# Kernel optimization log

Measured on AMD Instinct MI355X. Metric: run time of the kernel, lower is better.

The kernel has to match this reference:

```python
import jax, jax.numpy as jnp
import numpy as np


def setup_inputs() -> dict:
    key = jax.random.key(0)
    ks = jax.random.split(key, 7)
    B, T, D, H, L, O = 64, 512, 1024, 1024, 4, 256
    s = 1.0 / np.sqrt(H)
    return {
        "x": jax.random.normal(ks[0], (B, T, D), dtype=jnp.float32),
        "Wih": jax.random.normal(ks[1], (L, 4 * H, D), dtype=jnp.float32) * s,
        "Whh": jax.random.normal(ks[2], (L, 4 * H, H), dtype=jnp.float32) * s,
        "bih": jax.random.normal(ks[3], (L, 4 * H), dtype=jnp.float32) * s,
        "bhh": jax.random.normal(ks[4], (L, 4 * H), dtype=jnp.float32) * s,
        "fc_w": jax.random.normal(ks[5], (O, H), dtype=jnp.float32) * s,
        "fc_b": jax.random.normal(ks[6], (O,), dtype=jnp.float32) * s,
    }


def reference(x, Wih, Whh, bih, bhh, fc_w, fc_b):
    B, T, D = x.shape
    L, fourH, H = Whh.shape[0], Whh.shape[1], Whh.shape[2]

    def step(carry, xt):
        h, c = carry  # each [L, B, H]
        inp = xt      # [B, D]
        new_h, new_c = [], []
        for i in range(L):  # fixed small layer loop
            gates = (inp @ Wih[i].T + bih[i] + h[i] @ Whh[i].T + bhh[i])  # [B, 4H]
            ig, fg, gg, og = jnp.split(gates, 4, axis=-1)
            ig, fg, og = jax.nn.sigmoid(ig), jax.nn.sigmoid(fg), jax.nn.sigmoid(og)
            gg = jnp.tanh(gg)
            ci = fg * c[i] + ig * gg
            hi = og * jnp.tanh(ci)
            new_h.append(hi)
            new_c.append(ci)
            inp = hi
        return (jnp.stack(new_h), jnp.stack(new_c)), None

    h0 = jnp.zeros((L, B, H), dtype=x.dtype)
    c0 = jnp.zeros((L, B, H), dtype=x.dtype)
    xt_seq = jnp.swapaxes(x, 0, 1)  # [T, B, D]
    (h, c), _ = jax.lax.scan(step, (h0, c0), xt_seq)
    return h[-1] @ fc_w.T + fc_b  # [B, O]
```

## Files before the change

### kernel.cpp

```cpp
#include <hip/hip_runtime.h>
#include <stdint.h>

typedef __attribute__((ext_vector_type(8))) short short8;
typedef __attribute__((ext_vector_type(4))) float floatx4;
typedef unsigned short ushort_t;

#define NB 256
#define NT 512
constexpr int B_ = 64, T_ = 512, D_ = 1024, H_ = 1024, O_ = 256;

constexpr size_t WS_SLOTS = 0;
constexpr size_t WS_MODE  = 4096;
constexpr size_t WS_HBUF  = 8192;
constexpr size_t WS_NEED  = WS_HBUF + (size_t)4*4*B_*H_*2;

constexpr int LDS_BYTES = 131072;

__device__ __forceinline__ float bs2f(ushort_t s){
  union { unsigned u; float f; } v; v.u = ((unsigned)s) << 16; return v.f;
}
__device__ __forceinline__ ushort_t f2bs(float f){
  union { float f; unsigned u; } v; v.f = f;
  unsigned r = (v.u + 0x7fffu + ((v.u >> 16) & 1u)) >> 16;
  return (ushort_t)r;
}
__device__ __forceinline__ float sigf(float x){ return 1.f/(1.f + __expf(-x)); }
__device__ __forceinline__ float tanh_f(float x){ return 1.f - 2.f/(__expf(2.f*x) + 1.f); }
__device__ __forceinline__ short8 ldb8(const ushort_t* p){ return *(const short8*)p; }
__device__ __forceinline__ short8 cvt8v(const float* p){
  floatx4 a = *(const floatx4*)p;
  floatx4 b = *(const floatx4*)(p + 4);
  short8 r;
  #pragma unroll
  for (int j = 0; j < 4; ++j){ r[j] = (short)f2bs(a[j]); r[j+4] = (short)f2bs(b[j]); }
  return r;
}

__device__ __forceinline__ void waitge_sys(unsigned* p, int tgt){
  while ((int)__hip_atomic_load(p, __ATOMIC_RELAXED, __HIP_MEMORY_SCOPE_SYSTEM) < tgt)
    __builtin_amdgcn_s_sleep(2);
  asm volatile("" ::: "memory");
}
__device__ __forceinline__ void st_dword_sys(void* p, unsigned v){
  asm volatile("global_store_dword %0, %1, off sc0 sc1"
               :: "v"((uintptr_t)p), "v"(v) : "memory");
}
template<int AUX>
__device__ __forceinline__ void gl2lds16(const void* g, void* l){
  __builtin_amdgcn_global_load_lds(
      (const __attribute__((address_space(1))) unsigned*)g,
      (__attribute__((address_space(3))) unsigned*)l, 16, 0, AUX);
}

__global__ void sniff_init(const ushort_t* __restrict__ fcb_u,
                           unsigned* __restrict__ slots, unsigned* __restrict__ mode){
  __shared__ int cnt;
  if (threadIdx.x == 0) cnt = 0;
  __syncthreads();
  slots[threadIdx.x] = 0u;
  unsigned u = fcb_u[threadIdx.x];
  unsigned e = (u >> 7) & 0xFFu;
  if (e >= 0x89u) atomicAdd(&cnt, 1);
  __syncthreads();
  if (threadIdx.x == 0) *mode = (cnt >= 4) ? 1u : 0u;
}

__global__ __launch_bounds__(NT, 2)
void lstm_pipe(const void* __restrict__ xv,   const void* __restrict__ Wihv,
               const void* __restrict__ Whhv, const void* __restrict__ bihv,
               const void* __restrict__ bhhv, const void* __restrict__ fcwv,
               const void* __restrict__ fcbv, void* __restrict__ outv,
               ushort_t* __restrict__ hbuf, unsigned* __restrict__ slots,
               const unsigned* __restrict__ modep)
{
  extern __shared__ char lds_raw[];
  const int tid  = threadIdx.x;
  const int bx   = blockIdx.x;
  const int lane = tid & 63;
  const int wv   = tid >> 6;
  const int q    = lane >> 4;
  const int l15  = lane & 15;
  const int wg   = wv >> 1;
  const int kh   = wv & 1;
  const int s7   = l15 & 7;
  const int layer = bx >> 6;
  const int slice = bx & 63;
  const int jbase = slice * 16;

  const unsigned md = *modep;
  const bool f32in  = (md == 1u);
  const float*    xF = (const float*)xv;
  const ushort_t* xB = (const ushort_t*)xv;

  short8 wih_r[16], whh_r[16];
  {
    const size_t wrow = (size_t)layer*4*H_ + (size_t)wg*H_ + jbase + l15;
    const size_t koff = (size_t)kh*512 + q*8;
    if (f32in){
      const float* wi = (const float*)Wihv + wrow*D_ + koff;
      const float* wh = (const float*)Whhv + wrow*H_ + koff;
      #pragma unroll
      for (int kk = 0; kk < 16; ++kk){
        wih_r[kk] = cvt8v(wi + kk*32);
        whh_r[kk] = cvt8v(wh + kk*32);
      }
    } else {
      const ushort_t* wi = (const ushort_t*)Wihv + wrow*D_ + koff;
      const ushort_t* wh = (const ushort_t*)Whhv + wrow*H_ + koff;
      #pragma unroll
      for (int kk = 0; kk < 16; ++kk){
        wih_r[kk] = ldb8(wi + kk*32);
        whh_r[kk] = ldb8(wh + kk*32);
      }
    }
  }

  const int pb = tid >> 3;
  const int pj = tid & 7;
  float bsum[4][2];
  {
    #pragma unroll
    for (int g = 0; g < 4; ++g){
      const size_t idx = (size_t)layer*4*H_ + (size_t)g*H_ + jbase + 2*pj;
      if (f32in){
        bsum[g][0] = ((const float*)bihv)[idx]   + ((const float*)bhhv)[idx];
        bsum[g][1] = ((const float*)bihv)[idx+1] + ((const float*)bhhv)[idx+1];
      } else {
        bsum[g][0] = bs2f(((const ushort_t*)bihv)[idx])   + bs2f(((const ushort_t*)bhhv)[idx]);
        bsum[g][1] = bs2f(((const ushort_t*)bihv)[idx+1]) + bs2f(((const ushort_t*)bhhv)[idx+1]);
      }
    }
  }
  float c2[2] = {0.f, 0.f};

  #define GEMM_STEP(WREG) do {                                                 \
    const short8* Ap_ = (const short8*)lds_raw;                                \
    _Pragma("unroll")                                                          \
    for (int kk = 0; kk < 16; ++kk){                                           \
      const int csw = ((kh<<6) + q + (kk<<2)) ^ s7;                            \
      short8 a0 = Ap_[(size_t)(l15+ 0)*128 + csw];                             \
      short8 a1 = Ap_[(size_t)(l15+16)*128 + csw];                             \
      short8 a2 = Ap_[(size_t)(l15+32)*128 + csw];                             \
      short8 a3 = Ap_[(size_t)(l15+48)*128 + csw];                             \
      acc[0] = __builtin_amdgcn_mfma_f32_16x16x32_bf16(a0, WREG[kk], acc[0], 0,0,0); \
      acc[1] = __builtin_amdgcn_mfma_f32_16x16x32_bf16(a1, WREG[kk], acc[1], 0,0,0); \
      acc[2] = __builtin_amdgcn_mfma_f32_16x16x32_bf16(a2, WREG[kk], acc[2], 0,0,0); \
      acc[3] = __builtin_amdgcn_mfma_f32_16x16x32_bf16(a3, WREG[kk], acc[3], 0,0,0); \
    }                                                                          \
  } while(0)

  for (int t = 0; t < T_; ++t){
    if (t > 0 && tid < 64)                    waitge_sys(&slots[layer*64 + tid], t + 1);
    if (layer < 3 && t >= 3 && tid >= 64 && tid < 128)
                                              waitge_sys(&slots[(layer+1)*64 + (tid-64)], t - 2);
    __syncthreads();

    floatx4 acc[4];
    #pragma unroll
    for (int mt = 0; mt < 4; ++mt) acc[mt] = floatx4{0.f,0.f,0.f,0.f};

    if (t > 0){
      const char* src = (const char*)(hbuf + ((size_t)layer*4 + ((t+3)&3))*(size_t)(B_*H_));
      #pragma unroll
      for (int it = 0; it < 16; ++it){
        const int d = it*NT + tid;
        const int r = d >> 7, c = d & 127, cc = c ^ (r & 7);
        gl2lds16<0x11>(src + (size_t)r*2048 + (size_t)cc*16, lds_raw + (size_t)d*16);
      }
      asm volatile("s_waitcnt vmcnt(0)" ::: "memory");
      __syncthreads();
      GEMM_STEP(whh_r);
    }

    if (layer > 0 && tid < 64) waitge_sys(&slots[(layer-1)*64 + tid], t + 2);
    __syncthreads();

    if (layer == 0){
      if (f32in){
        #pragma unroll 4
        for (int it = 0; it < 16; ++it){
          const int d = it*NT + tid;
          const int r = d >> 7, c = d & 127, cc = c ^ (r & 7);
          const float* sp = xF + ((size_t)r*T_ + t)*D_ + (size_t)cc*8;
          floatx4 A0 = *(const floatx4*)sp, A1 = *(const floatx4*)(sp + 4);
          short8 v;
          #pragma unroll
          for (int j2 = 0; j2 < 4; ++j2){ v[j2] = (short)f2bs(A0[j2]); v[j2+4] = (short)f2bs(A1[j2]); }
          *(short8*)(lds_raw + (size_t)d*16) = v;
        }
      } else {
        const char* srcx = (const char*)xB;
        #pragma unroll
        for (int it = 0; it < 16; ++it){
          const int d = it*NT + tid;
          const int r = d >> 7, c = d & 127, cc = c ^ (r & 7);
          gl2lds16<0>(srcx + (((size_t)r*T_ + t)*D_ + (size_t)cc*8)*2, lds_raw + (size_t)d*16);
        }
      }
    } else {
      const char* srch = (const char*)(hbuf + ((size_t)(layer-1)*4 + (t&3))*(size_t)(B_*H_));
      #pragma unroll
      for (int it = 0; it < 16; ++it){
        const int d = it*NT + tid;
        const int r = d >> 7, c = d & 127, cc = c ^ (r & 7);
        gl2lds16<0x11>(srch + (size_t)r*2048 + (size_t)cc*16, lds_raw + (size_t)d*16);
      }
    }
    asm volatile("s_waitcnt vmcnt(0)" ::: "memory");
    __syncthreads();
    GEMM_STEP(wih_r);
    __syncthreads();

    {
      float* xch = (float*)lds_raw;
      #pragma unroll
      for (int mt = 0; mt < 4; ++mt)
        #pragma unroll
        for (int r = 0; r < 4; ++r)
          xch[((size_t)(wg*2 + kh)*64 + mt*16 + q*4 + r)*18 + l15] = acc[mt][r];
    }
    __syncthreads();

    {
      const float* xch = (const float*)lds_raw;
      float hv[2];
      #pragma unroll
      for (int u = 0; u < 2; ++u){
        const int j = 2*pj + u;
        #define XG(g) (xch[((size_t)((g)*2+0)*64 + pb)*18 + j] + xch[((size_t)((g)*2+1)*64 + pb)*18 + j])
        float ig = sigf  (XG(0) + bsum[0][u]);
        float fg = sigf  (XG(1) + bsum[1][u]);
        float gg = tanh_f(XG(2) + bsum[2][u]);
        float og = sigf  (XG(3) + bsum[3][u]);
        #undef XG
        float cn = fg*c2[u] + ig*gg;
        c2[u] = cn;
        hv[u] = og*tanh_f(cn);
      }
      unsigned pack = (unsigned)f2bs(hv[0]) | ((unsigned)f2bs(hv[1]) << 16);
      ushort_t* hw = hbuf + ((size_t)layer*4 + (t&3))*(size_t)(B_*H_) + (size_t)pb*H_ + jbase + 2*pj;
      st_dword_sys(hw, pack);
    }
    asm volatile("s_waitcnt vmcnt(0)" ::: "memory");
    __syncthreads();
    if (tid == 0)
      __hip_atomic_store(&slots[layer*64 + slice], (unsigned)(t + 2),
                         __ATOMIC_RELAXED, __HIP_MEMORY_SCOPE_SYSTEM);
  }

  if (bx < B_){
    if (tid < 64) waitge_sys(&slots[3*64 + tid], T_ + 1);
    __syncthreads();
    const char* hr = (const char*)(hbuf + (((size_t)3*4 + ((T_-1)&3))*B_ + bx)*(size_t)H_);
    if (tid < 128) gl2lds16<0x11>(hr + (size_t)tid*16, lds_raw + (size_t)tid*16);
    asm volatile("s_waitcnt vmcnt(0)" ::: "memory");
    __syncthreads();
    if (tid < O_){
      const int b = bx, o = tid;
      const short8* hh = (const short8*)lds_raw;
      if (f32in){
        float acc = ((const float*)fcbv)[o];
        const float* wr = (const float*)fcwv + (size_t)o*H_;
        for (int k8 = 0; k8 < H_/8; ++k8){
          short8 h8 = hh[k8];
          #pragma unroll
          for (int u = 0; u < 8; ++u) acc += bs2f((ushort_t)h8[u]) * wr[k8*8 + u];
        }
        ((float*)outv)[(size_t)b*O_ + o] = acc;
      } else {
        float acc = bs2f(((const ushort_t*)fcbv)[o]);
        const ushort_t* wr = (const ushort_t*)fcwv + (size_t)o*H_;
        for (int k8 = 0; k8 < H_/8; ++k8){
          short8 h8 = hh[k8];
          short8 w8 = ldb8(wr + k8*8);
          #pragma unroll
          for (int u = 0; u < 8; ++u) acc += bs2f((ushort_t)h8[u]) * bs2f((ushort_t)w8[u]);
        }
        ((ushort_t*)outv)[(size_t)b*O_ + o] = f2bs(acc);
      }
    }
  }
  #undef GEMM_STEP
}

extern "C" void kernel_launch(void* const* d_in, const int* in_sizes, int n_in,
                              void* d_out, int out_size, void* d_ws, size_t ws_size,
                              hipStream_t stream){
  static bool attr_done = false;
  if (!attr_done){
    hipFuncSetAttribute(reinterpret_cast<const void*>(&lstm_pipe),
                        hipFuncAttributeMaxDynamicSharedMemorySize, LDS_BYTES);
    attr_done = true;
  }
  char* ws = (char*)d_ws;
  unsigned* slots = (unsigned*)(ws + WS_SLOTS);
  unsigned* mode  = (unsigned*)(ws + WS_MODE);
  ushort_t* hbuf  = (ushort_t*)(ws + WS_HBUF);

  sniff_init<<<1, 256, 0, stream>>>((const ushort_t*)d_in[6], slots, mode);
  lstm_pipe<<<NB, NT, LDS_BYTES, stream>>>(d_in[0], d_in[1], d_in[2], d_in[3], d_in[4],
                                           d_in[5], d_in[6], d_out, hbuf, slots, mode);
}
```

Baseline: 11.47 ms.

## Load h operands straight from global into registers, split K across all waves

Each of the 8 waves now owns a 128-wide K slice across all four gates, not a (gate, K-half) pair. Activation fragments are read directly from hbuf and x into registers with system-scope atomic loads, replacing staging through LDS. Partial sums from all waves are reduced in LDS before the gate math, and all dependency waits happen together at the top of each step. This removes the LDS staging copies and extra barriers per timestep, at the cost of an 8-way LDS reduction, more LDS, and uncached system-scope global loads on the critical path.

```diff
diff --git a/kernel.cpp b/kernel.cpp
--- a/kernel.cpp
+++ b/kernel.cpp
@@ -3,7 +3,9 @@
 
 typedef __attribute__((ext_vector_type(8))) short short8;
 typedef __attribute__((ext_vector_type(4))) float floatx4;
+typedef __attribute__((ext_vector_type(2))) float float2v;
 typedef unsigned short ushort_t;
+typedef unsigned long long ull_t;
 
 #define NB 256
 #define NT 512
@@ -12,9 +14,8 @@
 constexpr size_t WS_SLOTS = 0;
 constexpr size_t WS_MODE  = 4096;
 constexpr size_t WS_HBUF  = 8192;
-constexpr size_t WS_NEED  = WS_HBUF + (size_t)4*4*B_*H_*2;
-
-constexpr int LDS_BYTES = 131072;
+
+constexpr int LDS_BYTES = 147456;
 
 __device__ __forceinline__ float bs2f(ushort_t s){
   union { unsigned u; float f; } v; v.u = ((unsigned)s) << 16; return v.f;
@@ -27,13 +28,15 @@
 __device__ __forceinline__ float sigf(float x){ return 1.f/(1.f + __expf(-x)); }
 __device__ __forceinline__ float tanh_f(float x){ return 1.f - 2.f/(__expf(2.f*x) + 1.f); }
 __device__ __forceinline__ short8 ldb8(const ushort_t* p){ return *(const short8*)p; }
-__device__ __forceinline__ short8 cvt8v(const float* p){
-  floatx4 a = *(const floatx4*)p;
-  floatx4 b = *(const floatx4*)(p + 4);
-  short8 r;
-  #pragma unroll
-  for (int j = 0; j < 4; ++j){ r[j] = (short)f2bs(a[j]); r[j+4] = (short)f2bs(b[j]); }
-  return r;
+
+__device__ __forceinline__ unsigned cvtpk(float lo, float hi){
+  unsigned r; asm("v_cvt_pk_bf16_f32 %0, %1, %2" : "=v"(r) : "v"(lo), "v"(hi)); return r;
+}
+__device__ __forceinline__ short8 cvt8pk(floatx4 a, floatx4 b){
+  union { unsigned u[4]; short8 s; } c;
+  c.u[0] = cvtpk(a[0], a[1]); c.u[1] = cvtpk(a[2], a[3]);
+  c.u[2] = cvtpk(b[0], b[1]); c.u[3] = cvtpk(b[2], b[3]);
+  return c.s;
 }
 
 __device__ __forceinline__ void waitge_sys(unsigned* p, int tgt){
@@ -77,12 +80,9 @@
   const int tid  = threadIdx.x;
   const int bx   = blockIdx.x;
   const int lane = tid & 63;
-  const int wv   = tid >> 6;
+  const int w    = tid >> 6;
   const int q    = lane >> 4;
   const int l15  = lane & 15;
-  const int wg   = wv >> 1;
-  const int kh   = wv & 1;
-  const int s7   = l15 & 7;
   const int layer = bx >> 6;
   const int slice = bx & 63;
   const int jbase = slice * 16;
@@ -92,25 +92,23 @@
   const float*    xF = (const float*)xv;
   const ushort_t* xB = (const ushort_t*)xv;
 
-  short8 wih_r[16], whh_r[16];
+  short8 wih_r[4][4], whh_r[4][4];
   {
-    const size_t wrow = (size_t)layer*4*H_ + (size_t)wg*H_ + jbase + l15;
-    const size_t koff = (size_t)kh*512 + q*8;
-    if (f32in){
-      const float* wi = (const float*)Wihv + wrow*D_ + koff;
-      const float* wh = (const float*)Whhv + wrow*H_ + koff;
-      #pragma unroll
-      for (int kk = 0; kk < 16; ++kk){
-        wih_r[kk] = cvt8v(wi + kk*32);
-        whh_r[kk] = cvt8v(wh + kk*32);
-      }
-    } else {
-      const ushort_t* wi = (const ushort_t*)Wihv + wrow*D_ + koff;
-      const ushort_t* wh = (const ushort_t*)Whhv + wrow*H_ + koff;
-      #pragma unroll
-      for (int kk = 0; kk < 16; ++kk){
-        wih_r[kk] = ldb8(wi + kk*32);
-        whh_r[kk] = ldb8(wh + kk*32);
+    #pragma unroll
+    for (int g = 0; g < 4; ++g){
+      const size_t row = (size_t)layer*4*H_ + (size_t)g*H_ + jbase + l15;
+      #pragma unroll
+      for (int kl = 0; kl < 4; ++kl){
+        const size_t koff = (size_t)w*128 + kl*32 + q*8;
+        if (f32in){
+          const float* wi = (const float*)Wihv + row*D_ + koff;
+          const float* wh = (const float*)Whhv + row*H_ + koff;
+          wih_r[g][kl] = cvt8pk(*(const floatx4*)wi, *(const floatx4*)(wi+4));
+          whh_r[g][kl] = cvt8pk(*(const floatx4*)wh, *(const floatx4*)(wh+4));
+        } else {
+          wih_r[g][kl] = ldb8((const ushort_t*)Wihv + row*D_ + koff);
+          whh_r[g][kl] = ldb8((const ushort_t*)Whhv + row*H_ + koff);
+        }
       }
     }
   }
@@ -133,112 +131,134 @@
   }
   float c2[2] = {0.f, 0.f};
 
-  #define GEMM_STEP(WREG) do {                                                 \
-    const short8* Ap_ = (const short8*)lds_raw;                                \
+  const size_t u0 = (size_t)l15*256 + (size_t)w*32 + (size_t)q*2;
+
+  union AFu { ull_t u[2]; short8 s; };
+
+  #define LD2(BUF, BASE, MH, KL) do {                                          \
     _Pragma("unroll")                                                          \
-    for (int kk = 0; kk < 16; ++kk){                                           \
-      const int csw = ((kh<<6) + q + (kk<<2)) ^ s7;                            \
-      short8 a0 = Ap_[(size_t)(l15+ 0)*128 + csw];                             \
-      short8 a1 = Ap_[(size_t)(l15+16)*128 + csw];                             \
-      short8 a2 = Ap_[(size_t)(l15+32)*128 + csw];                             \
-      short8 a3 = Ap_[(size_t)(l15+48)*128 + csw];                             \
-      acc[0] = __builtin_amdgcn_mfma_f32_16x16x32_bf16(a0, WREG[kk], acc[0], 0,0,0); \
-      acc[1] = __builtin_amdgcn_mfma_f32_16x16x32_bf16(a1, WREG[kk], acc[1], 0,0,0); \
-      acc[2] = __builtin_amdgcn_mfma_f32_16x16x32_bf16(a2, WREG[kk], acc[2], 0,0,0); \
-      acc[3] = __builtin_amdgcn_mfma_f32_16x16x32_bf16(a3, WREG[kk], acc[3], 0,0,0); \
-    }                                                                          \
+    for (int mt_ = 0; mt_ < 2; ++mt_){                                         \
+      const ull_t* p_ = (BASE) + (size_t)(MH)*8192 + (size_t)mt_*4096          \
+                               + u0 + (size_t)(KL)*8;                          \
+      (BUF)[mt_].u[0] = __hip_atomic_load(p_,   __ATOMIC_RELAXED, __HIP_MEMORY_SCOPE_SYSTEM); \
+      (BUF)[mt_].u[1] = __hip_atomic_load(p_+1, __ATOMIC_RELAXED, __HIP_MEMORY_SCOPE_SYSTEM); \
+    } } while(0)
+
+  #define MF2(BUF, WR, KL) do {                                                \
+    _Pragma("unroll")                                                          \
+    for (int g_ = 0; g_ < 4; ++g_)                                             \
+      _Pragma("unroll")                                                        \
+      for (int mt_ = 0; mt_ < 2; ++mt_)                                        \
+        acc[g_][mt_] = __builtin_amdgcn_mfma_f32_16x16x32_bf16(                \
+            (BUF)[mt_].s, (WR)[g_][(KL)], acc[g_][mt_], 0, 0, 0);              \
   } while(0)
 
   for (int t = 0; t < T_; ++t){
     if (t > 0 && tid < 64)                    waitge_sys(&slots[layer*64 + tid], t + 1);
-    if (layer < 3 && t >= 3 && tid >= 64 && tid < 128)
-                                              waitge_sys(&slots[(layer+1)*64 + (tid-64)], t - 2);
-    __syncthreads();
-
-    floatx4 acc[4];
+    if (layer > 0 && tid >= 64 && tid < 128)  waitge_sys(&slots[(layer-1)*64 + (tid-64)], t + 2);
+    if (layer < 3 && t >= 3 && tid >= 128 && tid < 192)
+                                              waitge_sys(&slots[(layer+1)*64 + (tid-128)], t - 2);
+    __syncthreads();
+
+    float* xch = (float*)lds_raw;
+    const int wb = w*4608 + q*72 + l15;
+
     #pragma unroll
-    for (int mt = 0; mt < 4; ++mt) acc[mt] = floatx4{0.f,0.f,0.f,0.f};
-
-    if (t > 0){
-      const char* src = (const char*)(hbuf + ((size_t)layer*4 + ((t+3)&3))*(size_t)(B_*H_));
-      #pragma unroll
-      for (int it = 0; it < 16; ++it){
-        const int d = it*NT + tid;
-        const int r = d >> 7, c = d & 127, cc = c ^ (r & 7);
-        gl2lds16<0x11>(src + (size_t)r*2048 + (size_t)cc*16, lds_raw + (size_t)d*16);
-      }
-      asm volatile("s_waitcnt vmcnt(0)" ::: "memory");
-      __syncthreads();
-      GEMM_STEP(whh_r);
-    }
-
-    if (layer > 0 && tid < 64) waitge_sys(&slots[(layer-1)*64 + tid], t + 2);
-    __syncthreads();
-
-    if (layer == 0){
-      if (f32in){
-        #pragma unroll 4
-        for (int it = 0; it < 16; ++it){
-          const int d = it*NT + tid;
-          const int r = d >> 7, c = d & 127, cc = c ^ (r & 7);
-          const float* sp = xF + ((size_t)r*T_ + t)*D_ + (size_t)cc*8;
-          floatx4 A0 = *(const floatx4*)sp, A1 = *(const floatx4*)(sp + 4);
-          short8 v;
-          #pragma unroll
-          for (int j2 = 0; j2 < 4; ++j2){ v[j2] = (short)f2bs(A0[j2]); v[j2+4] = (short)f2bs(A1[j2]); }
-          *(short8*)(lds_raw + (size_t)d*16) = v;
+    for (int mh = 0; mh < 2; ++mh){
+      floatx4 acc[4][2];
+      #pragma unroll
+      for (int g = 0; g < 4; ++g)
+        #pragma unroll
+        for (int mt = 0; mt < 2; ++mt) acc[g][mt] = floatx4{0.f,0.f,0.f,0.f};
+
+      if (t > 0){
+        const ull_t* hb = (const ull_t*)(hbuf + ((size_t)layer*4 + ((t+3)&3))*(size_t)(B_*H_));
+        AFu A0[2], A1[2];
+        LD2(A0, hb, mh, 0); LD2(A1, hb, mh, 1);
+        MF2(A0, whh_r, 0);  LD2(A0, hb, mh, 2);
+        MF2(A1, whh_r, 1);  LD2(A1, hb, mh, 3);
+        MF2(A0, whh_r, 2);
+        MF2(A1, whh_r, 3);
+      }
+
+      if (layer > 0){
+        const ull_t* ib = (const ull_t*)(hbuf + ((size_t)(layer-1)*4 + (t&3))*(size_t)(B_*H_));
+        AFu A0[2], A1[2];
+        LD2(A0, ib, mh, 0); LD2(A1, ib, mh, 1);
+        MF2(A0, wih_r, 0);  LD2(A0, ib, mh, 2);
+        MF2(A1, wih_r, 1);  LD2(A1, ib, mh, 3);
+        MF2(A0, wih_r, 2);
+        MF2(A1, wih_r, 3);
+      } else {
+        if (f32in){
+          const float* xp = xF + (size_t)(mh*32 + l15)*T_*D_ + (size_t)t*D_ + w*128 + q*8;
+          #pragma unroll
+          for (int kl = 0; kl < 4; ++kl){
+            short8 af[2];
+            #pragma unroll
+            for (int mt = 0; mt < 2; ++mt){
+              const float* p = xp + (size_t)mt*16*T_*D_ + kl*32;
+              af[mt] = cvt8pk(*(const floatx4*)p, *(const floatx4*)(p+4));
+            }
+            #pragma unroll
+            for (int g = 0; g < 4; ++g)
+              #pragma unroll
+              for (int mt = 0; mt < 2; ++mt)
+                acc[g][mt] = __builtin_amdgcn_mfma_f32_16x16x32_bf16(
+                    af[mt], wih_r[g][kl], acc[g][mt], 0, 0, 0);
+          }
+        } else {
+          const ushort_t* xp = xB + (size_t)(mh*32 + l15)*T_*D_ + (size_t)t*D_ + w*128 + q*8;
+          #pragma unroll
+          for (int kl = 0; kl < 4; ++kl){
+            short8 af[2];
+            #pragma unroll
+            for (int mt = 0; mt < 2; ++mt)
+              af[mt] = ldb8(xp + (size_t)mt*16*T_*D_ + kl*32);
+            #pragma unroll
+            for (int g = 0; g < 4; ++g)
+              #pragma unroll
+              for (int mt = 0; mt < 2; ++mt)
+                acc[g][mt] = __builtin_amdgcn_mfma_f32_16x16x32_bf16(
+                    af[mt], wih_r[g][kl], acc[g][mt], 0, 0, 0);
+          }
         }
-      } else {
-        const char* srcx = (const char*)xB;
+      }
+
+      #pragma unroll
+      for (int g = 0; g < 4; ++g)
         #pragma unroll
-        for (int it = 0; it < 16; ++it){
-          const int d = it*NT + tid;
-          const int r = d >> 7, c = d & 127, cc = c ^ (r & 7);
-          gl2lds16<0>(srcx + (((size_t)r*T_ + t)*D_ + (size_t)cc*8)*2, lds_raw + (size_t)d*16);
-        }
-      }
-    } else {
-      const char* srch = (const char*)(hbuf + ((size_t)(layer-1)*4 + (t&3))*(size_t)(B_*H_));
-      #pragma unroll
-      for (int it = 0; it < 16; ++it){
-        const int d = it*NT + tid;
-        const int r = d >> 7, c = d & 127, cc = c ^ (r & 7);
-        gl2lds16<0x11>(srch + (size_t)r*2048 + (size_t)cc*16, lds_raw + (size_t)d*16);
-      }
-    }
-    asm volatile("s_waitcnt vmcnt(0)" ::: "memory");
-    __syncthreads();
-    GEMM_STEP(wih_r);
+        for (int mt = 0; mt < 2; ++mt)
+          #pragma unroll
+          for (int r = 0; r < 4; ++r)
+            xch[wb + g*1152 + (mh*2 + mt)*288 + r*18] = acc[g][mt][r];
+    }
     __syncthreads();
 
     {
-      float* xch = (float*)lds_raw;
-      #pragma unroll
-      for (int mt = 0; mt < 4; ++mt)
+      const float* xchc = (const float*)lds_raw;
+      const int rb = pb*18 + 2*pj;
+      float2v s[4] = { float2v{0.f,0.f}, float2v{0.f,0.f}, float2v{0.f,0.f}, float2v{0.f,0.f} };
+      #pragma unroll
+      for (int w8 = 0; w8 < 8; ++w8)
         #pragma unroll
-        for (int r = 0; r < 4; ++r)
-          xch[((size_t)(wg*2 + kh)*64 + mt*16 + q*4 + r)*18 + l15] = acc[mt][r];
-    }
-    __syncthreads();
-
-    {
-      const float* xch = (const float*)lds_raw;
+        for (int g = 0; g < 4; ++g)
+          s[g] += *(const float2v*)&xchc[w8*4608 + g*1152 + rb];
+
       float hv[2];
       #pragma unroll
       for (int u = 0; u < 2; ++u){
-        const int j = 2*pj + u;
-        #define XG(g) (xch[((size_t)((g)*2+0)*64 + pb)*18 + j] + xch[((size_t)((g)*2+1)*64 + pb)*18 + j])
-        float ig = sigf  (XG(0) + bsum[0][u]);
-        float fg = sigf  (XG(1) + bsum[1][u]);
-        float gg = tanh_f(XG(2) + bsum[2][u]);
-        float og = sigf  (XG(3) + bsum[3][u]);
-        #undef XG
+        float ig = sigf  (s[0][u] + bsum[0][u]);
+        float fg = sigf  (s[1][u] + bsum[1][u]);
+        float gg = tanh_f(s[2][u] + bsum[2][u]);
+        float og = sigf  (s[3][u] + bsum[3][u]);
         float cn = fg*c2[u] + ig*gg;
         c2[u] = cn;
         hv[u] = og*tanh_f(cn);
       }
-      unsigned pack = (unsigned)f2bs(hv[0]) | ((unsigned)f2bs(hv[1]) << 16);
-      ushort_t* hw = hbuf + ((size_t)layer*4 + (t&3))*(size_t)(B_*H_) + (size_t)pb*H_ + jbase + 2*pj;
+      unsigned pack = cvtpk(hv[0], hv[1]);
+      ushort_t* hw = hbuf + ((size_t)layer*4 + (t&3))*(size_t)(B_*H_)
+                   + (size_t)pb*H_ + jbase + 2*pj;
       st_dword_sys(hw, pack);
     }
     asm volatile("s_waitcnt vmcnt(0)" ::: "memory");
@@ -247,6 +267,9 @@
       __hip_atomic_store(&slots[layer*64 + slice], (unsigned)(t + 2),
                          __ATOMIC_RELAXED, __HIP_MEMORY_SCOPE_SYSTEM);
   }
+
+  #undef LD2
+  #undef MF2
 
   if (bx < B_){
     if (tid < 64) waitge_sys(&slots[3*64 + tid], T_ + 1);
@@ -280,7 +303,6 @@
       }
     }
   }
-  #undef GEMM_STEP
 }
 
 extern "C" void kernel_launch(void* const* d_in, const int* in_sizes, int n_in,
```

Result: slower. 12.37 ms (+7.8%).
